# Kernel optimization log

Measured on AMD Instinct MI355X. Metric: run time of the kernel, lower is better.

The kernel has to match this reference:

```python
import jax, jax.numpy as jnp
import numpy as np
from jax import lax

NEG = -1e4
B, S, D, NL = 64, 512, 768, 9
L = NL + 2  # +start, +end states


def setup_inputs() -> dict:
    key = jax.random.key(0)
    ks = jax.random.split(key, 4)
    inputs = jax.random.normal(ks[0], (B, S, D), jnp.float32)
    predict_mask = jnp.ones((B, S), jnp.int32)
    labels = jax.random.randint(ks[1], (B, S), 0, NL)
    W = jax.random.normal(ks[2], (NL, D), jnp.float32) * 0.02
    b = jnp.zeros((NL,), jnp.float32)
    trans = jax.random.normal(ks[3], (L, L), jnp.float32) * 0.1  # trans[next, prev]
    return {"inputs": inputs, "predict_mask": predict_mask, "labels": labels,
            "W": W, "b": b, "trans": trans}


def crf_loss(inputs, predict_mask, labels, W, b, trans):
    Bs, Ss, _ = inputs.shape
    Ls = trans.shape[0]
    start, end = Ls - 2, Ls - 1
    # linear projection (dropout is identity in eval)
    logits = jnp.einsum('bsd,ld->bsl', inputs, W) + b  # [B,S,NL]
    # pad_logits: append -1e4 scores for start/end states
    logits = jnp.concatenate(
        [logits, jnp.full((Bs, Ss, 2), NEG, logits.dtype)], axis=-1)  # [B,S,L]
    lens = predict_mask.sum(-1)  # [B]

    # ---- calc_norm_score: forward algorithm (logsumexp DP over time) ----
    alpha0 = jnp.full((Bs, Ls), NEG, logits.dtype).at[:, start].set(0.0)

    def step(carry, logit_t):
        alpha, t = carry
        # mat[b, next, prev] = emit[b,next] + alpha[b,prev] + trans[next,prev]
        mat = logit_t[:, :, None] + alpha[:, None, :] + trans[None, :, :]
        alpha_nxt = jax.nn.logsumexp(mat, axis=2)
        alpha = jnp.where((t < lens)[:, None], alpha_nxt, alpha)
        return (alpha, t + 1), None

    (alpha, _), _ = lax.scan(step, (alpha0, jnp.int32(0)),
                             jnp.swapaxes(logits, 0, 1))
    norm = jax.nn.logsumexp(alpha + trans[end][None, :], axis=1)  # [B]

    # ---- calc_gold_score = unary + binary ----
    tok_mask = jnp.arange(Ss)[None, :] < lens[:, None]
    unary = jnp.take_along_axis(logits, labels[:, :, None], axis=2)[..., 0]
    unary = jnp.where(tok_mask, unary, 0.0).sum(1)  # [B]

    labels_ext = jnp.concatenate(
        [jnp.full((Bs, 1), start, labels.dtype), labels,
         jnp.full((Bs, 1), end, labels.dtype)], axis=1)  # [B,S+2]
    ext_mask = jnp.arange(Ss + 2)[None, :] < (lens + 1)[:, None]
    labels_ext = jnp.where(ext_mask, labels_ext, end)
    trn_scr = trans[labels_ext[:, 1:], labels_ext[:, :-1]]  # [B,S+1]
    trn_mask = jnp.arange(Ss + 1)[None, :] < (lens + 1)[:, None]
    binary = jnp.where(trn_mask, trn_scr, 0.0).sum(1)  # [B]

    loglik = (unary + binary) - norm
    return -loglik.mean()


def reference(inputs, predict_mask, labels, W, b, trans):
    return crf_loss(inputs, predict_mask, labels, W, b, trans)
```

## Files before the change

kernel.cpp:

```cpp
#include <hip/hip_runtime.h>

#define Bc 64
#define Sc 512
#define Dc 768
#define NLc 9
#define Lc 11
#define START (Lc-2)
#define ENDL (Lc-1)
#define NEGC -10000.0f
#define LOG2E 1.4426950408889634f
#define LN2 0.6931471805599453f
#define CHUNK 16
#define NCH (Sc / CHUNK)
#define WROW 776

typedef __attribute__((ext_vector_type(8))) short s16x8;
typedef __attribute__((ext_vector_type(4))) float f32x4;

union U4 { float4 f; unsigned int u[4]; };
union R8 { unsigned int w[4]; s16x8 v; };

static __device__ __forceinline__ s16x8 pack8(float4 lo, float4 hi) {
  U4 L, H; L.f = lo; H.f = hi;
  R8 r;
  r.w[0] = (L.u[1] & 0xFFFF0000u) | (L.u[0] >> 16);
  r.w[1] = (L.u[3] & 0xFFFF0000u) | (L.u[2] >> 16);
  r.w[2] = (H.u[1] & 0xFFFF0000u) | (H.u[0] >> 16);
  r.w[3] = (H.u[3] & 0xFFFF0000u) | (H.u[2] >> 16);
  return r.v;
}

__global__ __launch_bounds__(256, 4) void k_logits(const float* __restrict__ x,
    const float* __restrict__ W, const float* __restrict__ bias,
    float* __restrict__ out)
{
  __shared__ unsigned short Wb[16][WROW];
  for (int i = threadIdx.x; i < 16 * 384; i += 256) {
    const int r = i / 384, c = i % 384;
    unsigned int w = 0u;
    if (r < NLc) {
      U4 t; t.f.x = W[r * Dc + 2 * c]; t.f.y = W[r * Dc + 2 * c + 1];
      w = (t.u[1] & 0xFFFF0000u) | (t.u[0] >> 16);
    }
    *reinterpret_cast<unsigned int*>(&Wb[r][2 * c]) = w;
  }
  __syncthreads();

  const int lane = threadIdx.x & 63;
  const int wid  = threadIdx.x >> 6;
  const int tile = blockIdx.x * 4 + wid;
  const int R    = tile * 16;
  const int j    = lane & 15;
  const int kg   = lane >> 4;

  const float* xp = x + (size_t)(R + j) * Dc + kg * 8;
  const unsigned short* wrow = &Wb[j][kg * 8];

  f32x4 acc = {0.f, 0.f, 0.f, 0.f};
  float4 a0 = *reinterpret_cast<const float4*>(xp);
  float4 a1 = *reinterpret_cast<const float4*>(xp + 4);
  float4 b0 = *reinterpret_cast<const float4*>(xp + 32);
  float4 b1 = *reinterpret_cast<const float4*>(xp + 36);

#pragma unroll
  for (int t = 0; t < 24; ++t) {
    float4 n0, n1;
    if (t < 22) {
      n0 = *reinterpret_cast<const float4*>(xp + 32 * (t + 2));
      n1 = *reinterpret_cast<const float4*>(xp + 32 * (t + 2) + 4);
    }
    const s16x8 afrag = pack8(a0, a1);
    const s16x8 bfrag = *reinterpret_cast<const s16x8*>(wrow + 32 * t);
    acc = __builtin_amdgcn_mfma_f32_16x16x32_bf16(afrag, bfrag, acc, 0, 0, 0);
    a0 = b0; a1 = b1;
    if (t < 22) { b0 = n0; b1 = n1; }
  }

  if (j < NLc) {
    const float bb = bias[j];
#pragma unroll
    for (int r = 0; r < 4; ++r) {
      const int row = R + kg * 4 + r;
      out[(size_t)row * NLc + j] = acc[r] + bb;
    }
  }
}

__global__ __launch_bounds__(64) void k_chunk(const float* __restrict__ logits,
    const int* __restrict__ mask, const float* __restrict__ trans,
    float* __restrict__ Mout, unsigned* __restrict__ cnt)
{
  if (blockIdx.x == 0 && threadIdx.x == 0) cnt[0] = 0u;
  const int b = blockIdx.x / NCH;
  const int c = blockIdx.x % NCH;
  const int lane = threadIdx.x;
  __shared__ float Mbuf[2][121];
  __shared__ float Llog[CHUNK][NLc];

  int len = 0;
  for (int t = lane; t < Sc; t += 64) len += mask[b * Sc + t];
#pragma unroll
  for (int off = 32; off >= 1; off >>= 1) len += __shfl_xor(len, off);

  for (int i = lane; i < CHUNK * NLc; i += 64) {
    const int t = i / NLc, l = i % NLc;
    Llog[t][l] = logits[((size_t)b * Sc + c * CHUNK + t) * NLc + l];
  }
  for (int e = lane; e < 121; e += 64) {
    const int i = e % Lc, j = e / Lc;
    Mbuf[0][e] = (i == j) ? 0.f : NEGC;
  }
  const int e1 = lane;          const bool v1 = (e1 < 121);
  const int e2 = lane + 64;     const bool v2 = (e2 < 121);
  const int i1 = v1 ? (e1 % Lc) : 0, j1 = v1 ? (e1 / Lc) : 0;
  const int i2 = v2 ? (e2 % Lc) : 0, j2 = v2 ? (e2 / Lc) : 0;
  float trow1[Lc], trow2[Lc];
#pragma unroll
  for (int k = 0; k < Lc; k++) {
    trow1[k] = trans[i1 * Lc + k];
    trow2[k] = trans[i2 * Lc + k];
  }
  __syncthreads();

  int p = 0;
  for (int t = 0; t < CHUNK; ++t) {
    const int tg = c * CHUNK + t;
    if (tg < len) {
      const float lg1 = (i1 < NLc) ? Llog[t][i1] : NEGC;
      const float lg2 = (i2 < NLc) ? Llog[t][i2] : NEGC;
      float terms[Lc];
      float m1 = -3.0e38f;
#pragma unroll
      for (int k = 0; k < Lc; k++) {
        terms[k] = trow1[k] + Mbuf[p][j1 * Lc + k];
        m1 = fmaxf(m1, terms[k]);
      }
      float s1 = 0.f;
#pragma unroll
      for (int k = 0; k < Lc; k++) s1 += exp2f((terms[k] - m1) * LOG2E);
      const float n1 = lg1 + m1 + log2f(s1) * LN2;
      float m2 = -3.0e38f;
#pragma unroll
      for (int k = 0; k < Lc; k++) {
        terms[k] = trow2[k] + Mbuf[p][j2 * Lc + k];
        m2 = fmaxf(m2, terms[k]);
      }
      float s2 = 0.f;
#pragma unroll
      for (int k = 0; k < Lc; k++) s2 += exp2f((terms[k] - m2) * LOG2E);
      const float n2 = lg2 + m2 + log2f(s2) * LN2;
      if (v1) Mbuf[p ^ 1][e1] = n1;
      if (v2) Mbuf[p ^ 1][e2] = n2;
      p ^= 1;
    }
    __syncthreads();
  }
  for (int e = lane; e < 121; e += 64)
    Mout[((size_t)b * NCH + c) * 121 + e] = Mbuf[p][e];
}

__global__ __launch_bounds__(256) void k_batch(const float* __restrict__ logits,
    const int* __restrict__ mask, const int* __restrict__ labels,
    const float* __restrict__ trans, const float* __restrict__ Min,
    float* __restrict__ part, unsigned* __restrict__ cnt,
    float* __restrict__ out)
{
  const int b = blockIdx.x;
  const int tid = threadIdx.x;
  const int wid = tid >> 6;
  const int lane = tid & 63;
  const int sl = lane & 15;
  __shared__ float Ms[NCH * 121];
  __shared__ int   ls[4];
  __shared__ float fs[4];
  __shared__ int   len_sh;
  __shared__ float norm_sh;
  __shared__ int   do_final;

  {
    const float4* src = reinterpret_cast<const float4*>(Min + (size_t)b * NCH * 121);
    for (int i = tid; i < (NCH * 121) / 4; i += 256)
      reinterpret_cast<float4*>(Ms)[i] = src[i];
  }
  int lp = 0;
  for (int t = tid; t < Sc; t += 256) lp += mask[b * Sc + t];
#pragma unroll
  for (int off = 32; off >= 1; off >>= 1) lp += __shfl_down(lp, off);
  if (lane == 0) ls[wid] = lp;
  __syncthreads();
  if (tid == 0) len_sh = ls[0] + ls[1] + ls[2] + ls[3];
  __syncthreads();
  const int len = len_sh;

  if (wid == 0) {
    const int ii = (sl < Lc) ? sl : 0;
    float alpha = (sl == START) ? 0.f : NEGC;
#pragma unroll 1
    for (int c = 0; c < NCH; ++c) {
      const float* M = Ms + c * 121;
      float terms[Lc];
      float m = -3.0e38f;
#pragma unroll
      for (int k = 0; k < Lc; k++) {
        const float ak = __shfl(alpha, k, 16);
        terms[k] = M[k * Lc + ii] + ak;
        m = fmaxf(m, terms[k]);
      }
      float s = 0.f;
#pragma unroll
      for (int k = 0; k < Lc; k++) s += exp2f((terms[k] - m) * LOG2E);
      const float anew = m + log2f(s) * LN2;
      alpha = (sl < Lc) ? anew : alpha;
    }
    float v = (sl < Lc) ? (alpha + trans[ENDL * Lc + sl]) : -3.0e38f;
    float mm = v;
#pragma unroll
    for (int off = 8; off >= 1; off >>= 1) mm = fmaxf(mm, __shfl_xor(mm, off, 16));
    float se = exp2f((v - mm) * LOG2E);
#pragma unroll
    for (int off = 8; off >= 1; off >>= 1) se += __shfl_xor(se, off, 16);
    if (lane == 0) norm_sh = mm + log2f(se) * LN2;
  } else {
    float u = 0.f;
    for (int t = tid - 64; t < Sc; t += 192)
      if (t < len) u += logits[((size_t)b * Sc + t) * NLc + labels[b * Sc + t]];
    for (int t = tid - 64; t <= Sc; t += 192) {
      if (t <= len) {
        const int cur = (t == 0) ? START : ((t - 1 < len) ? labels[b * Sc + t - 1] : ENDL);
        const int nxt = (t < len) ? labels[b * Sc + t] : ENDL;
        u += trans[nxt * Lc + cur];
      }
    }
#pragma unroll
    for (int off = 32; off >= 1; off >>= 1) u += __shfl_down(u, off);
    if (lane == 0) fs[wid] = u;
  }
  __syncthreads();

  if (tid == 0) {
    const float pb = fs[1] + fs[2] + fs[3] - norm_sh;
    __hip_atomic_store(&part[b], pb, __ATOMIC_RELEASE, __HIP_MEMORY_SCOPE_AGENT);
    const unsigned old = __hip_atomic_fetch_add(cnt, 1u, __ATOMIC_ACQ_REL,
                                                __HIP_MEMORY_SCOPE_AGENT);
    do_final = (old == (unsigned)(Bc - 1)) ? 1 : 0;
  }
  __syncthreads();
  if (do_final && wid == 0) {
    float v = __hip_atomic_load(&part[lane], __ATOMIC_RELAXED,
                                __HIP_MEMORY_SCOPE_AGENT);
#pragma unroll
    for (int off = 32; off >= 1; off >>= 1) v += __shfl_xor(v, off);
    if (lane == 0) out[0] = -v * (1.0f / Bc);
  }
}

extern "C" void kernel_launch(void* const* d_in, const int* in_sizes, int n_in,
                              void* d_out, int out_size, void* d_ws, size_t ws_size,
                              hipStream_t stream)
{
  const float* x      = (const float*)d_in[0];
  const int*   mask   = (const int*)d_in[1];
  const int*   labels = (const int*)d_in[2];
  const float* W      = (const float*)d_in[3];
  const float* bias   = (const float*)d_in[4];
  const float* trans  = (const float*)d_in[5];
  float* out = (float*)d_out;
  float* ws  = (float*)d_ws;

  float*    ws_logits = ws;
  float*    ws_M      = ws_logits + (size_t)Bc * Sc * NLc;
  float*    ws_part   = ws_M + (size_t)Bc * NCH * 121;
  unsigned* ws_cnt    = (unsigned*)(ws_part + Bc);

  hipLaunchKernelGGL(k_logits, dim3(512), dim3(256), 0, stream, x, W, bias, ws_logits);
  hipLaunchKernelGGL(k_chunk,  dim3(Bc * NCH), dim3(64), 0, stream, ws_logits, mask, trans, ws_M, ws_cnt);
  hipLaunchKernelGGL(k_batch,  dim3(Bc), dim3(256), 0, stream, ws_logits, mask, labels, trans, ws_M, ws_part, ws_cnt, out);
}
```

Before: 63.92 us.

## Stage input rows into LDS via async global_load_lds double-buffering in logits GEMM

The projection kernel now copies 64-row by 96-column chunks of the activations straight into XOR-swizzled shared memory with global_load_lds. The copies are double-buffered across 8 K-chunks, so each 256-thread block handles 64 rows instead of each wave streaming its own rows from global memory through registers. The goal is better coalescing and overlap of HBM loads with the MFMA work. In exchange it uses more LDS, which lowers occupancy to 2 blocks per SM, and it adds barriers and hand-written vmcnt waits that depend on the load count per stage.

```diff
diff --git a/kernel.cpp b/kernel.cpp
--- a/kernel.cpp
+++ b/kernel.cpp
@@ -14,6 +14,12 @@
 #define NCH (Sc / CHUNK)
 #define WROW 776
 
+#define ROWS 64
+#define KC 96
+#define NKC 8
+#define XROW_B 384
+#define STG 6
+
 typedef __attribute__((ext_vector_type(8))) short s16x8;
 typedef __attribute__((ext_vector_type(4))) float f32x4;
 
@@ -30,12 +36,32 @@
   return r.v;
 }
 
-__global__ __launch_bounds__(256, 4) void k_logits(const float* __restrict__ x,
+__global__ __launch_bounds__(256, 2) void k_logits(const float* __restrict__ x,
     const float* __restrict__ W, const float* __restrict__ bias,
     float* __restrict__ out)
 {
+  __shared__ float Xb[2][ROWS * KC];
   __shared__ unsigned short Wb[16][WROW];
-  for (int i = threadIdx.x; i < 16 * 384; i += 256) {
+
+  const int tid = threadIdx.x;
+  const int Rb  = blockIdx.x * ROWS;
+
+#define STAGE(c, p)                                                            \
+  {                                                                            \
+    _Pragma("unroll")                                                          \
+    for (int u = 0; u < STG; ++u) {                                            \
+      const int lo   = (u * 256 + tid) * 16;        \
+      const int row  = lo / XROW_B;                                            \
+      const int colb = lo % XROW_B;                                            \
+      const int scol = colb ^ ((row & 7) << 4);    \
+      const float* gp = x + (size_t)(Rb + row) * Dc + (c) * KC + (scol >> 2);  \
+      __builtin_amdgcn_global_load_lds(gp, &Xb[p][0] + (lo >> 2), 16, 0, 0);   \
+    }                                                                          \
+  }
+  STAGE(0, 0)
+  STAGE(1, 1)
+
+  for (int i = tid; i < 16 * 384; i += 256) {
     const int r = i / 384, c = i % 384;
     unsigned int w = 0u;
     if (r < NLc) {
@@ -46,38 +72,43 @@
   }
   __syncthreads();
 
-  const int lane = threadIdx.x & 63;
-  const int wid  = threadIdx.x >> 6;
-  const int tile = blockIdx.x * 4 + wid;
-  const int R    = tile * 16;
+  const int lane = tid & 63;
+  const int w    = tid >> 6;
   const int j    = lane & 15;
   const int kg   = lane >> 4;
-
-  const float* xp = x + (size_t)(R + j) * Dc + kg * 8;
-  const unsigned short* wrow = &Wb[j][kg * 8];
+  const int sw   = (j & 7) << 4;
 
   f32x4 acc = {0.f, 0.f, 0.f, 0.f};
-  float4 a0 = *reinterpret_cast<const float4*>(xp);
-  float4 a1 = *reinterpret_cast<const float4*>(xp + 4);
-  float4 b0 = *reinterpret_cast<const float4*>(xp + 32);
-  float4 b1 = *reinterpret_cast<const float4*>(xp + 36);
-
-#pragma unroll
-  for (int t = 0; t < 24; ++t) {
-    float4 n0, n1;
-    if (t < 22) {
-      n0 = *reinterpret_cast<const float4*>(xp + 32 * (t + 2));
-      n1 = *reinterpret_cast<const float4*>(xp + 32 * (t + 2) + 4);
-    }
-    const s16x8 afrag = pack8(a0, a1);
-    const s16x8 bfrag = *reinterpret_cast<const s16x8*>(wrow + 32 * t);
-    acc = __builtin_amdgcn_mfma_f32_16x16x32_bf16(afrag, bfrag, acc, 0, 0, 0);
-    a0 = b0; a1 = b1;
-    if (t < 22) { b0 = n0; b1 = n1; }
-  }
+
+#pragma unroll
+  for (int c = 0; c < NKC; ++c) {
+    const int p = c & 1;
+    asm volatile("" ::: "memory");
+    const char* xrow = reinterpret_cast<const char*>(&Xb[p][(w * 16 + j) * KC]);
+#pragma unroll
+    for (int s = 0; s < 3; ++s) {
+      const int cb0 = (s * 128 + kg * 32) ^ sw;
+      const float4 a0 = *reinterpret_cast<const float4*>(xrow + cb0);
+      const float4 a1 = *reinterpret_cast<const float4*>(xrow + (cb0 ^ 16));
+      const s16x8 afrag = pack8(a0, a1);
+      const s16x8 bfrag = *reinterpret_cast<const s16x8*>(&Wb[j][c * KC + s * 32 + kg * 8]);
+      acc = __builtin_amdgcn_mfma_f32_16x16x32_bf16(afrag, bfrag, acc, 0, 0, 0);
+    }
+    __builtin_amdgcn_s_barrier();
+    if (c + 2 < NKC) {
+      STAGE(c + 2, p)
+      asm volatile("s_waitcnt vmcnt(6)" ::: "memory");
+    } else {
+      asm volatile("s_waitcnt vmcnt(0)" ::: "memory");
+    }
+    __builtin_amdgcn_sched_barrier(0);
+    __builtin_amdgcn_s_barrier();
+  }
+#undef STAGE
 
   if (j < NLc) {
     const float bb = bias[j];
+    const int R = Rb + w * 16;
 #pragma unroll
     for (int r = 0; r < 4; ++r) {
       const int row = R + kg * 4 + r;
```

Result: no change. 62.99 us (-1.5%).

## Split logits GEMM K dimension across four waves with partial-sum buffers

Applied to the files above, without the earlier changes.

The projection kernel now splits the 768-wide reduction across four waves per 16-row tile. Each wave writes its partial logits into one of four separate workspace buffers, and only the first adds the bias. The downstream chunk and batch kernels sum the four partials on load. This is meant to shorten the serial MFMA/load chain per wave and expose more memory-level parallelism in the bandwidth-bound GEMM. In exchange it writes and re-reads four times as much intermediate logits data and uses four times the workspace.

```diff
diff --git a/kernel.cpp b/kernel.cpp
--- a/kernel.cpp
+++ b/kernel.cpp
@@ -13,6 +13,7 @@
 #define CHUNK 16
 #define NCH (Sc / CHUNK)
 #define WROW 776
+#define PSTRIDE ((size_t)Bc * Sc * NLc)
 
 typedef __attribute__((ext_vector_type(8))) short s16x8;
 typedef __attribute__((ext_vector_type(4))) float f32x4;
@@ -30,12 +31,13 @@
   return r.v;
 }
 
-__global__ __launch_bounds__(256, 4) void k_logits(const float* __restrict__ x,
+__global__ __launch_bounds__(512, 6) void k_logits(const float* __restrict__ x,
     const float* __restrict__ W, const float* __restrict__ bias,
-    float* __restrict__ out)
+    float* __restrict__ p0, float* __restrict__ p1,
+    float* __restrict__ p2, float* __restrict__ p3)
 {
   __shared__ unsigned short Wb[16][WROW];
-  for (int i = threadIdx.x; i < 16 * 384; i += 256) {
+  for (int i = threadIdx.x; i < 16 * 384; i += 512) {
     const int r = i / 384, c = i % 384;
     unsigned int w = 0u;
     if (r < NLc) {
@@ -46,15 +48,17 @@
   }
   __syncthreads();
 
-  const int lane = threadIdx.x & 63;
-  const int wid  = threadIdx.x >> 6;
-  const int tile = blockIdx.x * 4 + wid;
+  const int tid  = threadIdx.x;
+  const int lane = tid & 63;
+  const int wid  = tid >> 6;
+  const int tile = blockIdx.x * 2 + (wid >> 2);
+  const int h    = wid & 3;
   const int R    = tile * 16;
   const int j    = lane & 15;
   const int kg   = lane >> 4;
 
-  const float* xp = x + (size_t)(R + j) * Dc + kg * 8;
-  const unsigned short* wrow = &Wb[j][kg * 8];
+  const float* xp = x + (size_t)(R + j) * Dc + h * 192 + kg * 8;
+  const unsigned short* wrow = &Wb[j][h * 192 + kg * 8];
 
   f32x4 acc = {0.f, 0.f, 0.f, 0.f};
   float4 a0 = *reinterpret_cast<const float4*>(xp);
@@ -63,9 +67,9 @@
   float4 b1 = *reinterpret_cast<const float4*>(xp + 36);
 
 #pragma unroll
-  for (int t = 0; t < 24; ++t) {
+  for (int t = 0; t < 6; ++t) {
     float4 n0, n1;
-    if (t < 22) {
+    if (t < 4) {
       n0 = *reinterpret_cast<const float4*>(xp + 32 * (t + 2));
       n1 = *reinterpret_cast<const float4*>(xp + 32 * (t + 2) + 4);
     }
@@ -73,20 +77,23 @@
     const s16x8 bfrag = *reinterpret_cast<const s16x8*>(wrow + 32 * t);
     acc = __builtin_amdgcn_mfma_f32_16x16x32_bf16(afrag, bfrag, acc, 0, 0, 0);
     a0 = b0; a1 = b1;
-    if (t < 22) { b0 = n0; b1 = n1; }
+    if (t < 4) { b0 = n0; b1 = n1; }
   }
 
   if (j < NLc) {
-    const float bb = bias[j];
+    float* dst = (h == 0) ? p0 : (h == 1) ? p1 : (h == 2) ? p2 : p3;
+    const float bb = (h == 0) ? bias[j] : 0.f;
 #pragma unroll
     for (int r = 0; r < 4; ++r) {
       const int row = R + kg * 4 + r;
-      out[(size_t)row * NLc + j] = acc[r] + bb;
-    }
-  }
-}
-
-__global__ __launch_bounds__(64) void k_chunk(const float* __restrict__ logits,
+      dst[(size_t)row * NLc + j] = acc[r] + bb;
+    }
+  }
+}
+
+__global__ __launch_bounds__(64) void k_chunk(const float* __restrict__ p0,
+    const float* __restrict__ p1, const float* __restrict__ p2,
+    const float* __restrict__ p3,
     const int* __restrict__ mask, const float* __restrict__ trans,
     float* __restrict__ Mout, unsigned* __restrict__ cnt)
 {
@@ -104,7 +111,8 @@
 
   for (int i = lane; i < CHUNK * NLc; i += 64) {
     const int t = i / NLc, l = i % NLc;
-    Llog[t][l] = logits[((size_t)b * Sc + c * CHUNK + t) * NLc + l];
+    const size_t idx = ((size_t)b * Sc + c * CHUNK + t) * NLc + l;
+    Llog[t][l] = p0[idx] + p1[idx] + p2[idx] + p3[idx];
   }
   for (int e = lane; e < 121; e += 64) {
     const int i = e % Lc, j = e / Lc;
@@ -159,7 +167,9 @@
     Mout[((size_t)b * NCH + c) * 121 + e] = Mbuf[p][e];
 }
 
-__global__ __launch_bounds__(256) void k_batch(const float* __restrict__ logits,
+__global__ __launch_bounds__(256) void k_batch(const float* __restrict__ p0,
+    const float* __restrict__ p1, const float* __restrict__ p2,
+    const float* __restrict__ p3,
     const int* __restrict__ mask, const int* __restrict__ labels,
     const float* __restrict__ trans, const float* __restrict__ Min,
     float* __restrict__ part, unsigned* __restrict__ cnt,
@@ -223,7 +233,10 @@
   } else {
     float u = 0.f;
     for (int t = tid - 64; t < Sc; t += 192)
-      if (t < len) u += logits[((size_t)b * Sc + t) * NLc + labels[b * Sc + t]];
+      if (t < len) {
+        const size_t idx = ((size_t)b * Sc + t) * NLc + labels[b * Sc + t];
+        u += p0[idx] + p1[idx] + p2[idx] + p3[idx];
+      }
     for (int t = tid - 64; t <= Sc; t += 192) {
       if (t <= len) {
         const int cur = (t == 0) ? START : ((t - 1 < len) ? labels[b * Sc + t - 1] : ENDL);
@@ -267,12 +280,19 @@
   float* out = (float*)d_out;
   float* ws  = (float*)d_ws;
 
-  float*    ws_logits = ws;
-  float*    ws_M      = ws_logits + (size_t)Bc * Sc * NLc;
-  float*    ws_part   = ws_M + (size_t)Bc * NCH * 121;
-  unsigned* ws_cnt    = (unsigned*)(ws_part + Bc);
-
-  hipLaunchKernelGGL(k_logits, dim3(512), dim3(256), 0, stream, x, W, bias, ws_logits);
-  hipLaunchKernelGGL(k_chunk,  dim3(Bc * NCH), dim3(64), 0, stream, ws_logits, mask, trans, ws_M, ws_cnt);
-  hipLaunchKernelGGL(k_batch,  dim3(Bc), dim3(256), 0, stream, ws_logits, mask, labels, trans, ws_M, ws_part, ws_cnt, out);
-}
+  float*    ws_p0   = ws;
+  float*    ws_p1   = ws_p0 + PSTRIDE;
+  float*    ws_p2   = ws_p1 + PSTRIDE;
+  float*    ws_p3   = ws_p2 + PSTRIDE;
+  float*    ws_M    = ws_p3 + PSTRIDE;
+  float*    ws_part = ws_M + (size_t)Bc * NCH * 121;
+  unsigned* ws_cnt  = (unsigned*)(ws_part + Bc);
+
+  hipLaunchKernelGGL(k_logits, dim3(1024), dim3(512), 0, stream,
+                     x, W, bias, ws_p0, ws_p1, ws_p2, ws_p3);
+  hipLaunchKernelGGL(k_chunk,  dim3(Bc * NCH), dim3(64), 0, stream,
+                     ws_p0, ws_p1, ws_p2, ws_p3, mask, trans, ws_M, ws_cnt);
+  hipLaunchKernelGGL(k_batch,  dim3(Bc), dim3(256), 0, stream,
+                     ws_p0, ws_p1, ws_p2, ws_p3, mask, labels, trans, ws_M,
+                     ws_part, ws_cnt, out);
+}
```

After: 62.45 us. 2.3% less time.
